# Kernel optimization log

Measured on AMD Instinct MI355X. Metric: run time of the kernel, lower is better.

## Reference

```python
import jax, jax.numpy as jnp
import numpy as np


def _edt_one(mask):
    """Exact 2D Euclidean distance transform of one (H, W) binary map.

    Distance from each pixel to the nearest foreground (==1) pixel; 0 at
    foreground pixels (matches scipy-style distance_map_from_binary_matrix).
    Pass 1: 1D L1 distance along the width via forward/backward scans.
    Pass 2: exact lower-envelope min over rows (brute-force, vectorized).
    """
    H, W = mask.shape
    INF = jnp.float32(H + W)  # larger than any achievable distance
    g = jnp.where(mask > 0.5, jnp.float32(0.0), INF)  # (H, W)

    def step(carry, col):  # carry: (H,) running distance, col: (H,)
        d = jnp.minimum(col, carry + 1.0)
        return d, d

    init = jnp.full((H,), INF, dnp := jnp.float32)
    _, f = jax.lax.scan(step, init, g.T)           # (W, H) left-to-right
    _, b = jax.lax.scan(step, init, g.T[::-1])     # (W, H) right-to-left
    d1 = jnp.minimum(f, b[::-1]).T                 # (H, W) 1D distance along width

    ii = jnp.arange(H, dtype=jnp.float32)
    offs = (ii[:, None] - ii[None, :]) ** 2        # (H, H) squared row offsets
    # D2[i, j] = min_i' d1[i', j]^2 + (i - i')^2  -> intermediate (H, H, W)
    D2 = jnp.min(d1[None, :, :] ** 2 + offs[:, :, None], axis=1)
    return jnp.sqrt(D2)


def compute_distance_map(y_true):
    N, C, H, W = y_true.shape
    flat = y_true.reshape(N * C, H, W)
    dm = jax.lax.map(_edt_one, flat).reshape(N, C, H, W)  # sequential over N*C images
    return dm / jnp.float32(max(H, W) - 1)


def setup_inputs() -> dict:
    key = jax.random.key(0)
    k1, k2 = jax.random.split(key)
    y_pred = jax.random.normal(k1, (8, 2, 512, 512), dtype=jnp.float32)
    y_true = jax.random.randint(k2, (8, 2, 512, 512), 0, 2).astype(jnp.float32)
    return {"y_pred": y_pred, "y_true": y_true}


def reference(y_pred, y_true):
    # mode == 'multiclass', from_logits=True: log_softmax(dim=1).exp() == softmax
    p = jax.nn.softmax(y_pred, axis=1)
    sqe = (p - y_true) ** 2
    # torch version computes the map on CPU via numpy -> detached from autodiff
    dm = jax.lax.stop_gradient(compute_distance_map(y_true))
    loss = jnp.mean((1.0 + dm) * sqe, axis=(0, 2, 3))  # per-channel mean
    return loss.mean()
```

## Files before the change

### kernel.cpp

```cpp
#include <hip/hip_runtime.h>
#include <math.h>


#define H 512
#define W 512
#define NIMG 16
#define HW (H * W)
#define RW 5
#define SEG 16
#define HALO (SEG + 2 * RW)
#define JT 256
#define NBLK (NIMG * (H / SEG) * (W / JT))

static __device__ __forceinline__ float fast_exp2(float x) {
#if __has_builtin(__builtin_amdgcn_exp2f)
    return __builtin_amdgcn_exp2f(x);
#else
    return exp2f(x);
#endif
}
static __device__ __forceinline__ float fast_rcp(float x) {
#if __has_builtin(__builtin_amdgcn_rcpf)
    return __builtin_amdgcn_rcpf(x);
#else
    return 1.0f / x;
#endif
}

__global__ __launch_bounds__(256) void edt_rows_kernel(const float* __restrict__ yt,
                                                       float* __restrict__ d1sq) {
    int wid = blockIdx.x * 4 + (threadIdx.x >> 6);
    int lane = threadIdx.x & 63;
    int img = wid >> 9;
    int row = wid & (H - 1);

    const float* rp = yt + ((size_t)img * H + row) * W;
    int k0 = lane * 8;
    float4 va = *reinterpret_cast<const float4*>(rp + k0);
    float4 vb = *reinterpret_cast<const float4*>(rp + k0 + 4);
    float g[8] = { va.x, va.y, va.z, va.w, vb.x, vb.y, vb.z, vb.w };
    const float INF = 1024.0f;
    #pragma unroll
    for (int t = 0; t < 8; ++t) g[t] = (g[t] > 0.5f) ? 0.0f : INF;

    const float BIG = 3.0e38f;
    float pm[8], sm[8];

    float run = BIG;
    #pragma unroll
    for (int t = 0; t < 8; ++t) {
        run = fminf(run, g[t] - (float)(k0 + t));
        pm[t] = run;
    }
    float incl = run;
    #pragma unroll
    for (int d = 1; d < 64; d <<= 1) {
        float o = __shfl_up(incl, d);
        if (lane >= d) incl = fminf(incl, o);
    }
    float excl = __shfl_up(incl, 1);
    if (lane == 0) excl = BIG;

    run = BIG;
    #pragma unroll
    for (int t = 7; t >= 0; --t) {
        run = fminf(run, g[t] + (float)(k0 + t));
        sm[t] = run;
    }
    float incl2 = run;
    #pragma unroll
    for (int d = 1; d < 64; d <<= 1) {
        float o = __shfl_down(incl2, d);
        if (lane < 64 - d) incl2 = fminf(incl2, o);
    }
    float excl2 = __shfl_down(incl2, 1);
    if (lane == 63) excl2 = BIG;

    float out[8];
    #pragma unroll
    for (int t = 0; t < 8; ++t) {
        float kf = (float)(k0 + t);
        float f = kf + fminf(excl, pm[t]);
        float b = -kf + fminf(excl2, sm[t]);
        float d = fminf(f, b);
        out[t] = d * d;
    }
    float* op = d1sq + (size_t)img * HW + (size_t)row * W + k0;
    *reinterpret_cast<float4*>(op)     = make_float4(out[0], out[1], out[2], out[3]);
    *reinterpret_cast<float4*>(op + 4) = make_float4(out[4], out[5], out[6], out[7]);
}

__global__ __launch_bounds__(256) void edt_cols_loss_kernel(
        const float* __restrict__ yp, const float* __restrict__ yt,
        const float* __restrict__ d1sq, double* __restrict__ part) {
    __shared__ double wsum[4];

    const int tid  = threadIdx.x;
    const int lane = tid & 63;
    const int wv   = tid >> 6;
    const int j    = blockIdx.x * JT + tid;
    const int i0   = blockIdx.y * SEG;
    const int img  = blockIdx.z;
    const int bid  = (blockIdx.z * gridDim.y + blockIdx.y) * gridDim.x + blockIdx.x;

    const float BIG = 3.0e38f;
    const float* dp = d1sq + (size_t)img * HW;

    float w[HALO];
    #pragma unroll
    for (int k = 0; k < HALO; ++k) {
        int ip = i0 - RW + k;
        w[k] = (ip >= 0 && ip < H) ? dp[ip * W + j] : BIG;
    }

    float mn[SEG];
    #pragma unroll
    for (int m = 0; m < SEG; ++m) {
        float a1 = fminf(w[m + 4], w[m + 6]) + 1.0f;
        float a2 = fminf(w[m + 3], w[m + 7]) + 4.0f;
        float a3 = fminf(w[m + 2], w[m + 8]) + 9.0f;
        float a4 = fminf(w[m + 1], w[m + 9]) + 16.0f;
        float a5 = fminf(w[m + 0], w[m + 10]) + 25.0f;
        mn[m] = fminf(fminf(fminf(w[m + 5], a1), fminf(a2, a3)), fminf(a4, a5));
    }

    bool need = false;
    #pragma unroll
    for (int m = 0; m < SEG; ++m) need |= (mn[m] > 36.0f);
    if (__any(need)) {
        for (int ip = 0; ip < H; ++ip) {
            float v = dp[ip * W + j];
            #pragma unroll
            for (int m = 0; m < SEG; ++m) {
                int d = (i0 + m) - ip;
                mn[m] = fminf(mn[m], v + (float)(d * d));
            }
        }
    }

    const int n = img >> 1;
    const int c = img & 1;
    const float* ypc = yp + (size_t)(n * 2 + c) * HW;
    const float* ypo = yp + (size_t)(n * 2 + (1 - c)) * HW;
    const float* ytc = yt + (size_t)img * HW;
    const float LOG2E = 1.44269504088896340736f;

    double local = 0.0;
    #pragma unroll
    for (int m = 0; m < SEG; ++m) {
        int idx = (i0 + m) * W + j;
        float dmv = sqrtf(mn[m]) * (1.0f / 511.0f);
        float d  = ypo[idx] - ypc[idx];
        float e  = fast_exp2(d * LOG2E);
        float p  = fast_rcp(1.0f + e);
        float df = p - ytc[idx];
        local += (double)((1.0f + dmv) * (df * df));
    }

    #pragma unroll
    for (int d = 32; d > 0; d >>= 1) local += __shfl_down(local, d);
    if (lane == 0) wsum[wv] = local;
    __syncthreads();
    if (tid == 0)
        part[bid] = wsum[0] + wsum[1] + wsum[2] + wsum[3];
}

__global__ __launch_bounds__(256) void finalize_kernel(const double* __restrict__ part,
                                                       float* __restrict__ out) {
    __shared__ double ws[4];
    int t = threadIdx.x;
    double v = part[t] + part[t + 256] + part[t + 512] + part[t + 768];
    #pragma unroll
    for (int d = 32; d > 0; d >>= 1) v += __shfl_down(v, d);
    if ((t & 63) == 0) ws[t >> 6] = v;
    __syncthreads();
    if (t == 0)
        out[0] = (float)((ws[0] + ws[1] + ws[2] + ws[3]) / (double)(NIMG * HW));
}

extern "C" void kernel_launch(void* const* d_in, const int* in_sizes, int n_in,
                              void* d_out, int out_size, void* d_ws, size_t ws_size,
                              hipStream_t stream) {
    const float* y_pred = (const float*)d_in[0];
    const float* y_true = (const float*)d_in[1];
    float* out = (float*)d_out;

    double* part = (double*)d_ws;
    float*  d1sq = (float*)((char*)d_ws + 16384);

    edt_rows_kernel<<<dim3(NIMG * H / 4), 256, 0, stream>>>(y_true, d1sq);
    edt_cols_loss_kernel<<<dim3(W / JT, H / SEG, NIMG), 256, 0, stream>>>(
        y_pred, y_true, d1sq, part);
    finalize_kernel<<<1, 256, 0, stream>>>(part, out);
}
```

Before: 86.36 us.

## Process both channels per block to share logits and derive y_true from d1sq

Each column/loss block now handles both channels of a sample, so the two logit planes are loaded once and both softmax probabilities are computed from them. y_true is no longer read: it is recovered from d1sq being zero at foreground pixels. The change halves the grid to 512 blocks, doubles register usage per thread, and makes the brute-force fallback run for both channels whenever either needs it.

```diff
diff --git a/kernel.cpp b/kernel.cpp
--- a/kernel.cpp
+++ b/kernel.cpp
@@ -10,7 +10,7 @@
 #define SEG 16
 #define HALO (SEG + 2 * RW)
 #define JT 256
-#define NBLK (NIMG * (H / SEG) * (W / JT))
+#define NBLK (8 * (H / SEG) * (W / JT))
 
 static __device__ __forceinline__ float fast_exp2(float x) {
 #if __has_builtin(__builtin_amdgcn_exp2f)
@@ -91,8 +91,8 @@
 }
 
 __global__ __launch_bounds__(256) void edt_cols_loss_kernel(
-        const float* __restrict__ yp, const float* __restrict__ yt,
-        const float* __restrict__ d1sq, double* __restrict__ part) {
+        const float* __restrict__ yp, const float* __restrict__ d1sq,
+        double* __restrict__ part) {
     __shared__ double wsum[4];
 
     const int tid  = threadIdx.x;
@@ -100,61 +100,78 @@
     const int wv   = tid >> 6;
     const int j    = blockIdx.x * JT + tid;
     const int i0   = blockIdx.y * SEG;
-    const int img  = blockIdx.z;
+    const int n    = blockIdx.z;
     const int bid  = (blockIdx.z * gridDim.y + blockIdx.y) * gridDim.x + blockIdx.x;
 
     const float BIG = 3.0e38f;
-    const float* dp = d1sq + (size_t)img * HW;
-
-    float w[HALO];
+    const float* dp0 = d1sq + (size_t)(2 * n)     * HW;
+    const float* dp1 = d1sq + (size_t)(2 * n + 1) * HW;
+
+    float w0[HALO], w1[HALO];
     #pragma unroll
     for (int k = 0; k < HALO; ++k) {
         int ip = i0 - RW + k;
-        w[k] = (ip >= 0 && ip < H) ? dp[ip * W + j] : BIG;
-    }
-
-    float mn[SEG];
+        bool inb = (ip >= 0 && ip < H);
+        int off = ip * W + j;
+        w0[k] = inb ? dp0[off] : BIG;
+        w1[k] = inb ? dp1[off] : BIG;
+    }
+
+    float mn0[SEG], mn1[SEG];
     #pragma unroll
     for (int m = 0; m < SEG; ++m) {
-        float a1 = fminf(w[m + 4], w[m + 6]) + 1.0f;
-        float a2 = fminf(w[m + 3], w[m + 7]) + 4.0f;
-        float a3 = fminf(w[m + 2], w[m + 8]) + 9.0f;
-        float a4 = fminf(w[m + 1], w[m + 9]) + 16.0f;
-        float a5 = fminf(w[m + 0], w[m + 10]) + 25.0f;
-        mn[m] = fminf(fminf(fminf(w[m + 5], a1), fminf(a2, a3)), fminf(a4, a5));
+        float a1 = fminf(w0[m + 4], w0[m + 6]) + 1.0f;
+        float a2 = fminf(w0[m + 3], w0[m + 7]) + 4.0f;
+        float a3 = fminf(w0[m + 2], w0[m + 8]) + 9.0f;
+        float a4 = fminf(w0[m + 1], w0[m + 9]) + 16.0f;
+        float a5 = fminf(w0[m + 0], w0[m + 10]) + 25.0f;
+        mn0[m] = fminf(fminf(fminf(w0[m + 5], a1), fminf(a2, a3)), fminf(a4, a5));
+        float b1 = fminf(w1[m + 4], w1[m + 6]) + 1.0f;
+        float b2 = fminf(w1[m + 3], w1[m + 7]) + 4.0f;
+        float b3 = fminf(w1[m + 2], w1[m + 8]) + 9.0f;
+        float b4 = fminf(w1[m + 1], w1[m + 9]) + 16.0f;
+        float b5 = fminf(w1[m + 0], w1[m + 10]) + 25.0f;
+        mn1[m] = fminf(fminf(fminf(w1[m + 5], b1), fminf(b2, b3)), fminf(b4, b5));
     }
 
     bool need = false;
     #pragma unroll
-    for (int m = 0; m < SEG; ++m) need |= (mn[m] > 36.0f);
+    for (int m = 0; m < SEG; ++m) need |= (mn0[m] > 36.0f) | (mn1[m] > 36.0f);
     if (__any(need)) {
         for (int ip = 0; ip < H; ++ip) {
-            float v = dp[ip * W + j];
+            float v0 = dp0[ip * W + j];
+            float v1 = dp1[ip * W + j];
             #pragma unroll
             for (int m = 0; m < SEG; ++m) {
                 int d = (i0 + m) - ip;
-                mn[m] = fminf(mn[m], v + (float)(d * d));
+                float dd = (float)(d * d);
+                mn0[m] = fminf(mn0[m], v0 + dd);
+                mn1[m] = fminf(mn1[m], v1 + dd);
             }
         }
     }
 
-    const int n = img >> 1;
-    const int c = img & 1;
-    const float* ypc = yp + (size_t)(n * 2 + c) * HW;
-    const float* ypo = yp + (size_t)(n * 2 + (1 - c)) * HW;
-    const float* ytc = yt + (size_t)img * HW;
+    const float* x0p = yp + (size_t)(2 * n)     * HW;
+    const float* x1p = yp + (size_t)(2 * n + 1) * HW;
     const float LOG2E = 1.44269504088896340736f;
 
     double local = 0.0;
     #pragma unroll
     for (int m = 0; m < SEG; ++m) {
         int idx = (i0 + m) * W + j;
-        float dmv = sqrtf(mn[m]) * (1.0f / 511.0f);
-        float d  = ypo[idx] - ypc[idx];
-        float e  = fast_exp2(d * LOG2E);
-        float p  = fast_rcp(1.0f + e);
-        float df = p - ytc[idx];
-        local += (double)((1.0f + dmv) * (df * df));
+        float x0 = x0p[idx], x1 = x1p[idx];
+        float e01 = fast_exp2((x1 - x0) * LOG2E);
+        float p0  = fast_rcp(1.0f + e01);
+        float e10 = fast_exp2((x0 - x1) * LOG2E);
+        float p1  = fast_rcp(1.0f + e10);
+        float yt0 = (w0[m + RW] == 0.0f) ? 1.0f : 0.0f;
+        float yt1 = (w1[m + RW] == 0.0f) ? 1.0f : 0.0f;
+        float dm0 = sqrtf(mn0[m]) * (1.0f / 511.0f);
+        float dm1 = sqrtf(mn1[m]) * (1.0f / 511.0f);
+        float df0 = p0 - yt0;
+        float df1 = p1 - yt1;
+        local += (double)((1.0f + dm0) * (df0 * df0))
+               + (double)((1.0f + dm1) * (df1 * df1));
     }
 
     #pragma unroll
@@ -169,7 +186,7 @@
                                                        float* __restrict__ out) {
     __shared__ double ws[4];
     int t = threadIdx.x;
-    double v = part[t] + part[t + 256] + part[t + 512] + part[t + 768];
+    double v = part[t] + part[t + 256];
     #pragma unroll
     for (int d = 32; d > 0; d >>= 1) v += __shfl_down(v, d);
     if ((t & 63) == 0) ws[t >> 6] = v;
@@ -189,7 +206,7 @@
     float*  d1sq = (float*)((char*)d_ws + 16384);
 
     edt_rows_kernel<<<dim3(NIMG * H / 4), 256, 0, stream>>>(y_true, d1sq);
-    edt_cols_loss_kernel<<<dim3(W / JT, H / SEG, NIMG), 256, 0, stream>>>(
-        y_pred, y_true, d1sq, part);
+    edt_cols_loss_kernel<<<dim3(W / JT, H / SEG, 8), 256, 0, stream>>>(
+        y_pred, d1sq, part);
     finalize_kernel<<<1, 256, 0, stream>>>(part, out);
 }
```

Measured after the change: 86.88 us. No clear change (+0.6%).
